# Kernel optimization log

Hardware: AMD Instinct MI355X
Metric: run time of the kernel (lower is better)

## Reference

```python
import jax, jax.numpy as jnp
import numpy as np

N_NODES = 100_000
N_EDGES = 1_600_000
N_FEAT = 64
HIDDEN = 64
BIOPRINT = 2048
N_GRAPHS = 1024


def setup_inputs() -> dict:
    key = jax.random.key(0)
    ks = jax.random.split(key, 12)
    x = jax.random.normal(ks[0], (N_NODES, N_FEAT), jnp.float32)
    edge_index = jax.random.randint(ks[1], (2, N_EDGES), 0, N_NODES, dtype=jnp.int64)
    batch = jnp.sort(jax.random.randint(ks[2], (N_NODES,), 0, N_GRAPHS, dtype=jnp.int64))
    def lin(k, fan_in, fan_out):
        s = 1.0 / np.sqrt(fan_in)
        return jax.random.uniform(k, (fan_in, fan_out), jnp.float32, -s, s)
    W1 = lin(ks[3], N_FEAT, HIDDEN)
    b1 = jnp.zeros((HIDDEN,), jnp.float32)
    W2 = lin(ks[4], HIDDEN, HIDDEN)
    b2 = jnp.zeros((HIDDEN,), jnp.float32)
    W3 = lin(ks[5], HIDDEN, HIDDEN)
    b3 = jnp.zeros((HIDDEN,), jnp.float32)
    Wd = lin(ks[6], HIDDEN, BIOPRINT)
    bd = jax.random.uniform(ks[7], (BIOPRINT,), jnp.float32, -1.0 / np.sqrt(HIDDEN), 1.0 / np.sqrt(HIDDEN))
    return {"x": x, "edge_index": edge_index, "batch": batch,
            "W1": W1, "b1": b1, "W2": W2, "b2": b2, "W3": W3, "b3": b3,
            "Wd": Wd, "bd": bd}


def reference(x, edge_index, batch, W1, b1, W2, b2, W3, b3, Wd, bd):
    n = x.shape[0]
    src, dst = edge_index[0], edge_index[1]
    # GCN symmetric normalization with self-loops: deg = in-degree + 1
    ones_e = jnp.ones(src.shape[0], x.dtype)
    deg = jax.ops.segment_sum(ones_e, dst, num_segments=n) + 1.0
    dinv = jax.lax.rsqrt(deg)  # deg >= 1 always
    self_norm = (dinv * dinv)[:, None]
    edge_norm = (dinv[src] * dinv[dst])[:, None]

    def gcn_conv(h, W, b):
        hw = h @ W  # [N, out]
        agg = jax.ops.segment_sum(hw[src] * edge_norm, dst, num_segments=n)
        return agg + hw * self_norm + b  # self-loop handled analytically

    h = jax.nn.relu(gcn_conv(x, W1, b1))
    h = jax.nn.relu(gcn_conv(h, W2, b2))
    h = gcn_conv(h, W3, b3)

    # global_mean_pool over graph ids
    cnt = jax.ops.segment_sum(jnp.ones(n, x.dtype), batch, num_segments=N_GRAPHS)
    pooled = jax.ops.segment_sum(h, batch, num_segments=N_GRAPHS) / jnp.maximum(cnt, 1.0)[:, None]

    # dropout(p=0.5) is identity in eval mode
    logits = pooled @ Wd + bd
    probs = jax.nn.softmax(logits, axis=-1)
    return (probs >= 0.5).astype(x.dtype)
```

## Files before the change

kernel.cpp:

```cpp
#include <hip/hip_runtime.h>
#include <hip/hip_fp16.h>
#include <math.h>

#define N_NODES   100000
#define N_EDGES   1600000
#define N_FEAT    64
#define HIDDEN    64
#define BIOPRINT  2048
#define N_GRAPHS  1024

#define SENTINEL  N_NODES
#define ELL_STRIDE 64

#define N_E4 (N_EDGES / 4)
#define FILL_BLOCKS ((N_E4 + 255) / 256)
#define MM1_BLOCKS (N_NODES / 32)
#define GS_BLOCKS  5

#define XCD_SLICE 12500
#define CHUNK_SHIFT 15
#define CH4 (1 << (CHUNK_SHIFT - 2))
#define NC 49
#define SLOT_P 56
#define CNT_BLOCKS (8 * SLOT_P)
#define PREP_BLOCKS ((N_NODES + 255) / 256)

typedef unsigned short u16;
typedef unsigned char  u8;

__device__ __forceinline__ __half2 shx_h2(__half2 v, int m) {
    int x = __shfl_xor(*(int*)&v, m);
    return *(__half2*)&x;
}

__device__ __forceinline__ void stage_w_perm(const float* __restrict__ W, float* sW, int t) {
    const float4* W4 = (const float4*)W;
    for (int i = t; i < 1024; i += 256) {
        float4 w = W4[i];
        int k = i >> 4;
        int c4 = (i & 15) * 4;
        int base = (k >> 2) * 256 + (k & 3);
        sW[base + (c4 + 0) * 4] = w.x;
        sW[base + (c4 + 1) * 4] = w.y;
        sW[base + (c4 + 2) * 4] = w.z;
        sW[base + (c4 + 3) * 4] = w.w;
    }
}

__global__ __launch_bounds__(256) void k_countmm(
        const int* __restrict__ dst, u16* __restrict__ counts, u8* __restrict__ rankl,
        const float* __restrict__ x, const float* __restrict__ W,
        __half* __restrict__ hw) {
    __shared__ int smem[XCD_SLICE];
    int bid = blockIdx.x, t = threadIdx.x;
    if (bid < CNT_BLOCKS) {
        int p = bid / SLOT_P;
        int c = bid % SLOT_P;
        if (c >= NC) return;
        int* hist = smem;
        for (int i = t; i < XCD_SLICE; i += 256) hist[i] = 0;
        __syncthreads();
        int lo = p * XCD_SLICE, hi = lo + XCD_SLICE;
        int base4 = c * CH4;
        int end4 = base4 + CH4; if (end4 > N_E4) end4 = N_E4;
        const int4* dst4 = (const int4*)dst;
        for (int i4 = base4 + t; i4 < end4; i4 += 256) {
            int4 d4 = dst4[i4];
            int e = i4 * 4;
            if (d4.x >= lo && d4.x < hi) rankl[e + 0] = (u8)atomicAdd(&hist[d4.x - lo], 1);
            if (d4.y >= lo && d4.y < hi) rankl[e + 1] = (u8)atomicAdd(&hist[d4.y - lo], 1);
            if (d4.z >= lo && d4.z < hi) rankl[e + 2] = (u8)atomicAdd(&hist[d4.z - lo], 1);
            if (d4.w >= lo && d4.w < hi) rankl[e + 3] = (u8)atomicAdd(&hist[d4.w - lo], 1);
        }
        __syncthreads();
        u16* crow = counts + (size_t)c * N_NODES + lo;
        for (int i = t; i < XCD_SLICE; i += 256) crow[i] = (u16)hist[i];
        return;
    }
    bid -= CNT_BLOCKS;
    float* sW = (float*)smem;
    float* sA = (float*)smem + 4096;
    stage_w_perm(W, sW, t);
    int row0 = bid * 32;
    ((float4*)sA)[t]       = ((const float4*)x)[row0 * 16 + t];
    ((float4*)sA)[t + 256] = ((const float4*)x)[row0 * 16 + t + 256];
    __syncthreads();
    int wave = t >> 6, lane = t & 63;
    const float4* sWp = (const float4*)sW;
    float sum[8] = {0.f, 0.f, 0.f, 0.f, 0.f, 0.f, 0.f, 0.f};
#pragma unroll
    for (int k4 = 0; k4 < 16; ++k4) {
        float4 w4 = sWp[k4 * 64 + lane];
#pragma unroll
        for (int hh = 0; hh < 8; ++hh) {
            float4 a4 = ((const float4*)&sA[(wave * 8 + hh) * 64])[k4];
            sum[hh] = fmaf(a4.x, w4.x, sum[hh]);
            sum[hh] = fmaf(a4.y, w4.y, sum[hh]);
            sum[hh] = fmaf(a4.z, w4.z, sum[hh]);
            sum[hh] = fmaf(a4.w, w4.w, sum[hh]);
        }
    }
#pragma unroll
    for (int hh = 0; hh < 8; ++hh) {
        int row = row0 + wave * 8 + hh;
        hw[(size_t)row * 64 + lane] = __float2half_rn(sum[hh]);
    }
}

__global__ __launch_bounds__(256) void k_prep(
        u16* __restrict__ counts, int* __restrict__ deg, float* __restrict__ dinv,
        const int* __restrict__ batch, int* __restrict__ gstart) {
    int bid = blockIdx.x, t = threadIdx.x;
    if (bid < PREP_BLOCKS) {
        int n = bid * 256 + t;
        if (n >= N_NODES) return;
        int s = 0;
#pragma unroll
        for (int c = 0; c < NC; ++c) {
            size_t idx = (size_t)c * N_NODES + n;
            int v = counts[idx];
            counts[idx] = (u16)s;
            s += v;
        }
        deg[n] = s;
        dinv[n] = rsqrtf((float)s + 1.0f);
        return;
    }
    int g = (bid - PREP_BLOCKS) * 256 + t;
    if (g > N_GRAPHS) return;
    if (g == N_GRAPHS) { gstart[g] = N_NODES; return; }
    int lo = 0, hi = N_NODES;
    while (lo < hi) { int mid = (lo + hi) >> 1; if (batch[mid] < g) lo = mid + 1; else hi = mid; }
    gstart[g] = lo;
}

__global__ __launch_bounds__(256) void k_fillscale(
        const int* __restrict__ src, const int* __restrict__ dst,
        const u8* __restrict__ rankl, const u16* __restrict__ counts,
        int* __restrict__ colELL,
        const int* __restrict__ deg, const float* __restrict__ dinv,
        __half* __restrict__ hw) {
    int bid = blockIdx.x, t = threadIdx.x;
    if (bid < FILL_BLOCKS) {
        int tid = bid * 256 + t;
        if (tid < N_E4) {
            int e = tid * 4;
            const u16* pref = counts + (size_t)(e >> CHUNK_SHIFT) * N_NODES;
            int4 d4 = ((const int4*)dst)[tid];
            uchar4 r4 = ((const uchar4*)rankl)[tid];
            int4 s4 = ((const int4*)src)[tid];
            int px = pref[d4.x] + r4.x; colELL[d4.x * ELL_STRIDE + (px & 63)] = s4.x;
            int py = pref[d4.y] + r4.y; colELL[d4.y * ELL_STRIDE + (py & 63)] = s4.y;
            int pz = pref[d4.z] + r4.z; colELL[d4.z * ELL_STRIDE + (pz & 63)] = s4.z;
            int pw = pref[d4.w] + r4.w; colELL[d4.w * ELL_STRIDE + (pw & 63)] = s4.w;
        }
        return;
    }
    bid -= FILL_BLOCKS;
    int row0 = bid * 32;
    int row = row0 + (t >> 3);
    float di = dinv[row];
    uint4* p = (uint4*)hw;
    uint4 v = p[(size_t)row * 8 + (t & 7)];
    __half2* h2 = (__half2*)&v;
#pragma unroll
    for (int c = 0; c < 4; ++c) {
        float2 f = __half22float2(h2[c]);
        h2[c] = __halves2half2(__float2half_rn(f.x * di), __float2half_rn(f.y * di));
    }
    p[(size_t)row * 8 + (t & 7)] = v;
    if (t < 32) {
        int r2 = row0 + t;
        int dv = deg[r2]; if (dv > 64) dv = 64;
        int vp = (dv + 15) & ~15;
        for (int j = dv; j < vp; ++j) colELL[r2 * ELL_STRIDE + j] = SENTINEL;
    }
}

__device__ __forceinline__ void gather2x8(
        const int* __restrict__ col, const uint4* __restrict__ hv,
        int rs, int re, int slot, int sub, float f[8]) {
    __half2 a0 = __float2half2_rn(0.f), a1 = a0, a2 = a0, a3 = a0;
    __half2 c0 = a0, c1 = a0, c2 = a0, c3 = a0;
    for (int e = rs; e < re; e += 16) {
        int s0 = __builtin_nontemporal_load(&col[e + slot]);
        int s1 = __builtin_nontemporal_load(&col[e + 2 + slot]);
        int s2 = __builtin_nontemporal_load(&col[e + 4 + slot]);
        int s3 = __builtin_nontemporal_load(&col[e + 6 + slot]);
        int s4 = __builtin_nontemporal_load(&col[e + 8 + slot]);
        int s5 = __builtin_nontemporal_load(&col[e + 10 + slot]);
        int s6 = __builtin_nontemporal_load(&col[e + 12 + slot]);
        int s7 = __builtin_nontemporal_load(&col[e + 14 + slot]);
        uint4 u0 = hv[(size_t)s0 * 8 + sub];
        uint4 u1 = hv[(size_t)s1 * 8 + sub];
        uint4 u2 = hv[(size_t)s2 * 8 + sub];
        uint4 u3 = hv[(size_t)s3 * 8 + sub];
        uint4 u4 = hv[(size_t)s4 * 8 + sub];
        uint4 u5 = hv[(size_t)s5 * 8 + sub];
        uint4 u6 = hv[(size_t)s6 * 8 + sub];
        uint4 u7 = hv[(size_t)s7 * 8 + sub];
        a0 = __hadd2(a0, *(__half2*)&u0.x); a1 = __hadd2(a1, *(__half2*)&u0.y);
        a2 = __hadd2(a2, *(__half2*)&u0.z); a3 = __hadd2(a3, *(__half2*)&u0.w);
        c0 = __hadd2(c0, *(__half2*)&u1.x); c1 = __hadd2(c1, *(__half2*)&u1.y);
        c2 = __hadd2(c2, *(__half2*)&u1.z); c3 = __hadd2(c3, *(__half2*)&u1.w);
        a0 = __hadd2(a0, *(__half2*)&u2.x); a1 = __hadd2(a1, *(__half2*)&u2.y);
        a2 = __hadd2(a2, *(__half2*)&u2.z); a3 = __hadd2(a3, *(__half2*)&u2.w);
        c0 = __hadd2(c0, *(__half2*)&u3.x); c1 = __hadd2(c1, *(__half2*)&u3.y);
        c2 = __hadd2(c2, *(__half2*)&u3.z); c3 = __hadd2(c3, *(__half2*)&u3.w);
        a0 = __hadd2(a0, *(__half2*)&u4.x); a1 = __hadd2(a1, *(__half2*)&u4.y);
        a2 = __hadd2(a2, *(__half2*)&u4.z); a3 = __hadd2(a3, *(__half2*)&u4.w);
        c0 = __hadd2(c0, *(__half2*)&u5.x); c1 = __hadd2(c1, *(__half2*)&u5.y);
        c2 = __hadd2(c2, *(__half2*)&u5.z); c3 = __hadd2(c3, *(__half2*)&u5.w);
        a0 = __hadd2(a0, *(__half2*)&u6.x); a1 = __hadd2(a1, *(__half2*)&u6.y);
        a2 = __hadd2(a2, *(__half2*)&u6.z); a3 = __hadd2(a3, *(__half2*)&u6.w);
        c0 = __hadd2(c0, *(__half2*)&u7.x); c1 = __hadd2(c1, *(__half2*)&u7.y);
        c2 = __hadd2(c2, *(__half2*)&u7.z); c3 = __hadd2(c3, *(__half2*)&u7.w);
    }
    a0 = __hadd2(a0, c0); a1 = __hadd2(a1, c1);
    a2 = __hadd2(a2, c2); a3 = __hadd2(a3, c3);
    a0 = __hadd2(a0, shx_h2(a0, 8));
    a1 = __hadd2(a1, shx_h2(a1, 8));
    a2 = __hadd2(a2, shx_h2(a2, 8));
    a3 = __hadd2(a3, shx_h2(a3, 8));
    float2 f0 = __half22float2(a0), f1 = __half22float2(a1);
    float2 f2 = __half22float2(a2), f3 = __half22float2(a3);
    f[0] = f0.x; f[1] = f0.y; f[2] = f1.x; f[3] = f1.y;
    f[4] = f2.x; f[5] = f2.y; f[6] = f3.x; f[7] = f3.y;
}

__global__ __launch_bounds__(256) void k_gmm(
        const int* __restrict__ deg, const int* __restrict__ col,
        const float* __restrict__ dinv, const float* __restrict__ b,
        const __half* __restrict__ hw_in, const float* __restrict__ W,
        __half* __restrict__ hw_out) {
    __shared__ float sW[64 * 64];
    __shared__ float sA[16 * 64];
    int t = threadIdx.x;
    stage_w_perm(W, sW, t);
    __syncthreads();

    int wave = t >> 6, lane = t & 63;
    int quarter = lane >> 4, slot = (lane >> 3) & 1, sub = lane & 7;
    int i0 = blockIdx.x * 16 + wave * 4;
    int i = i0 + quarter;
    float di = dinv[i];
    int dv = deg[i]; if (dv > 64) dv = 64;
    int rs = i * ELL_STRIDE;
    int re = rs + ((dv + 15) & ~15);
    const uint4* hv = (const uint4*)hw_in;

    float f[8];
    gather2x8(col, hv, rs, re, slot, sub, f);

    uint4 us = hv[(size_t)i * 8 + sub];
    float2 s0 = __half22float2(*(__half2*)&us.x);
    float2 s1 = __half22float2(*(__half2*)&us.y);
    float2 s2 = __half22float2(*(__half2*)&us.z);
    float2 s3 = __half22float2(*(__half2*)&us.w);
    float sf[8] = {s0.x, s0.y, s1.x, s1.y, s2.x, s2.y, s3.x, s3.y};
    float4 ba = ((const float4*)b)[sub * 2];
    float4 bb = ((const float4*)b)[sub * 2 + 1];
    float bf[8] = {ba.x, ba.y, ba.z, ba.w, bb.x, bb.y, bb.z, bb.w};
    if (slot == 0) {
        float r[8];
#pragma unroll
        for (int k = 0; k < 8; ++k) r[k] = fmaxf(fmaf(di, f[k] + sf[k], bf[k]), 0.f);
        *(float4*)&sA[(wave * 4 + quarter) * 64 + sub * 8]     = make_float4(r[0], r[1], r[2], r[3]);
        *(float4*)&sA[(wave * 4 + quarter) * 64 + sub * 8 + 4] = make_float4(r[4], r[5], r[6], r[7]);
    }

    const float4* sWp = (const float4*)sW;
    float sum[4] = {0.f, 0.f, 0.f, 0.f};
#pragma unroll
    for (int k4 = 0; k4 < 16; ++k4) {
        float4 w4 = sWp[k4 * 64 + lane];
#pragma unroll
        for (int hh = 0; hh < 4; ++hh) {
            float4 a4 = ((const float4*)&sA[(wave * 4 + hh) * 64])[k4];
            sum[hh] = fmaf(a4.x, w4.x, sum[hh]);
            sum[hh] = fmaf(a4.y, w4.y, sum[hh]);
            sum[hh] = fmaf(a4.z, w4.z, sum[hh]);
            sum[hh] = fmaf(a4.w, w4.w, sum[hh]);
        }
    }
#pragma unroll
    for (int hh = 0; hh < 4; ++hh)
        hw_out[(size_t)(i0 + hh) * 64 + lane] = __float2half_rn(sum[hh] * dinv[i0 + hh]);
}

__global__ __launch_bounds__(256) void k_gather3(
        const int* __restrict__ deg, const int* __restrict__ col,
        const float* __restrict__ dinv, const float* __restrict__ b,
        const __half* __restrict__ hw_in, __half* __restrict__ conv) {
    int t = threadIdx.x;
    int wave = t >> 6, lane = t & 63;
    int quarter = lane >> 4, slot = (lane >> 3) & 1, sub = lane & 7;
    int i = blockIdx.x * 16 + wave * 4 + quarter;
    float di = dinv[i];
    int dv = deg[i]; if (dv > 64) dv = 64;
    int rs = i * ELL_STRIDE;
    int re = rs + ((dv + 15) & ~15);
    const uint4* hv = (const uint4*)hw_in;

    float f[8];
    gather2x8(col, hv, rs, re, slot, sub, f);

    if (slot == 0) {
        uint4 us = hv[(size_t)i * 8 + sub];
        float2 s0 = __half22float2(*(__half2*)&us.x);
        float2 s1 = __half22float2(*(__half2*)&us.y);
        float2 s2 = __half22float2(*(__half2*)&us.z);
        float2 s3 = __half22float2(*(__half2*)&us.w);
        float sf[8] = {s0.x, s0.y, s1.x, s1.y, s2.x, s2.y, s3.x, s3.y};
        float4 ba = ((const float4*)b)[sub * 2];
        float4 bb = ((const float4*)b)[sub * 2 + 1];
        float bf[8] = {ba.x, ba.y, ba.z, ba.w, bb.x, bb.y, bb.z, bb.w};
        uint4 o;
        __half2* oh = (__half2*)&o;
#pragma unroll
        for (int c = 0; c < 4; ++c) {
            float r0 = fmaf(di, f[2 * c] + sf[2 * c], bf[2 * c]);
            float r1 = fmaf(di, f[2 * c + 1] + sf[2 * c + 1], bf[2 * c + 1]);
            oh[c] = __halves2half2(__float2half_rn(r0), __float2half_rn(r1));
        }
        ((uint4*)conv)[(size_t)i * 8 + sub] = o;
    }
}

__global__ __launch_bounds__(256) void k_dense(
        const __half* __restrict__ conv, const int* __restrict__ gstart,
        const float* __restrict__ Wd, const float* __restrict__ bd,
        float* __restrict__ out) {
    __shared__ float sred[4][64];
    __shared__ float sp[64];
    __shared__ float rmax[4];
    __shared__ float rsum[4];
    int t = threadIdx.x;
    int wave = t >> 6, lane = t & 63;
    int g = blockIdx.x;
    int n0 = gstart[g], n1 = gstart[g + 1];

    int fp = lane & 31;
    int par = lane >> 5;
    const __half2* conv2 = (const __half2*)conv;
    float2 acc2 = make_float2(0.f, 0.f);
    for (int i = n0 + wave * 2 + par; i < n1; i += 8) {
        float2 f = __half22float2(conv2[(size_t)i * 32 + fp]);
        acc2.x += f.x; acc2.y += f.y;
    }
    acc2.x += __shfl_xor(acc2.x, 32);
    acc2.y += __shfl_xor(acc2.y, 32);
    if (lane < 32) { sred[wave][2 * fp] = acc2.x; sred[wave][2 * fp + 1] = acc2.y; }
    __syncthreads();
    if (t < 64) {
        int n = n1 - n0;
        float s = sred[0][t] + sred[1][t] + sred[2][t] + sred[3][t];
        sp[t] = (n > 0) ? s / (float)n : 0.f;
    }
    __syncthreads();

    float acc[8];
#pragma unroll
    for (int r = 0; r < 8; ++r) acc[r] = bd[r * 256 + t];
    for (int k = 0; k < 64; ++k) {
        float h = sp[k];
#pragma unroll
        for (int r = 0; r < 8; ++r)
            acc[r] = fmaf(h, Wd[k * BIOPRINT + r * 256 + t], acc[r]);
    }

    float m = acc[0];
#pragma unroll
    for (int r = 1; r < 8; ++r) m = fmaxf(m, acc[r]);
#pragma unroll
    for (int off = 32; off > 0; off >>= 1) m = fmaxf(m, __shfl_xor(m, off));
    if (lane == 0) rmax[wave] = m;
    __syncthreads();
    m = fmaxf(fmaxf(rmax[0], rmax[1]), fmaxf(rmax[2], rmax[3]));

    float s = 0.f;
#pragma unroll
    for (int r = 0; r < 8; ++r) { acc[r] = expf(acc[r] - m); s += acc[r]; }
#pragma unroll
    for (int off = 32; off > 0; off >>= 1) s += __shfl_xor(s, off);
    if (lane == 0) rsum[wave] = s;
    __syncthreads();
    s = rsum[0] + rsum[1] + rsum[2] + rsum[3];

#pragma unroll
    for (int r = 0; r < 8; ++r) {
        float p = acc[r] / s;
        out[(size_t)g * BIOPRINT + r * 256 + t] = (p >= 0.5f) ? 1.0f : 0.0f;
    }
}


extern "C" void kernel_launch(void* const* d_in, const int* in_sizes, int n_in,
                              void* d_out, int out_size, void* d_ws, size_t ws_size,
                              hipStream_t stream) {
    const float* x     = (const float*)d_in[0];
    const int*   ei    = (const int*)d_in[1];
    const int*   batch = (const int*)d_in[2];
    const float* W1 = (const float*)d_in[3];
    const float* b1 = (const float*)d_in[4];
    const float* W2 = (const float*)d_in[5];
    const float* b2 = (const float*)d_in[6];
    const float* W3 = (const float*)d_in[7];
    const float* b3 = (const float*)d_in[8];
    const float* Wd = (const float*)d_in[9];
    const float* bd = (const float*)d_in[10];
    float* out = (float*)d_out;

    const int* src = ei;
    const int* dst = ei + N_EDGES;

    char* ws = (char*)d_ws;
    size_t off = 0;
    auto alloc = [&](size_t bytes) {
        void* p = ws + off;
        off += (bytes + 255) & ~(size_t)255;
        return p;
    };
    int*    deg    = (int*)alloc(N_NODES * sizeof(int));
    float*  dinv   = (float*)alloc(N_NODES * sizeof(float));
    u8*     rankl  = (u8*)alloc((size_t)N_EDGES * sizeof(u8));
    int*    gstart = (int*)alloc((N_GRAPHS + 1) * sizeof(int));
    u16*    counts = (u16*)alloc((size_t)NC * N_NODES * sizeof(u16));
    int*    colELL = (int*)alloc((size_t)N_NODES * ELL_STRIDE * sizeof(int));
    __half* bufA   = (__half*)alloc((size_t)(N_NODES + 1) * HIDDEN * sizeof(__half));
    __half* bufB   = (__half*)alloc((size_t)(N_NODES + 1) * HIDDEN * sizeof(__half));
    __half* conv   = (__half*)alloc((size_t)N_NODES * HIDDEN * sizeof(__half));

    hipMemsetAsync(bufA + (size_t)N_NODES * HIDDEN, 0, HIDDEN * sizeof(__half), stream);
    hipMemsetAsync(bufB + (size_t)N_NODES * HIDDEN, 0, HIDDEN * sizeof(__half), stream);

    k_countmm<<<CNT_BLOCKS + MM1_BLOCKS, 256, 0, stream>>>(dst, counts, rankl, x, W1, bufA);
    k_prep<<<PREP_BLOCKS + GS_BLOCKS, 256, 0, stream>>>(counts, deg, dinv, batch, gstart);
    k_fillscale<<<FILL_BLOCKS + MM1_BLOCKS, 256, 0, stream>>>(
        src, dst, rankl, counts, colELL, deg, dinv, bufA);

    const int g16_grid = N_NODES / 16;
    k_gmm<<<g16_grid, 256, 0, stream>>>(deg, colELL, dinv, b1, bufA, W2, bufB);
    k_gmm<<<g16_grid, 256, 0, stream>>>(deg, colELL, dinv, b2, bufB, W3, bufA);
    k_gather3<<<g16_grid, 256, 0, stream>>>(deg, colELL, dinv, b3, bufA, conv);
    k_dense<<<N_GRAPHS, 256, 0, stream>>>(conv, gstart, Wd, bd, out);
}
```

Before: 309.2 us.

## Partition ELL fill by XCD node slice with prefix offsets staged in LDS

```diff
diff --git a/kernel.cpp b/kernel.cpp
--- a/kernel.cpp
+++ b/kernel.cpp
@@ -13,7 +13,6 @@
 #define ELL_STRIDE 64
 
 #define N_E4 (N_EDGES / 4)
-#define FILL_BLOCKS ((N_E4 + 255) / 256)
 #define MM1_BLOCKS (N_NODES / 32)
 #define GS_BLOCKS  5
 
@@ -23,6 +22,7 @@
 #define NC 49
 #define SLOT_P 56
 #define CNT_BLOCKS (8 * SLOT_P)
+#define FILL_BLOCKS (8 * SLOT_P)
 #define PREP_BLOCKS ((N_NODES + 255) / 256)
 
 typedef unsigned short u16;
@@ -108,7 +108,8 @@
 }
 
 __global__ __launch_bounds__(256) void k_prep(
-        u16* __restrict__ counts, int* __restrict__ deg, float* __restrict__ dinv,
+        const u16* __restrict__ counts, u8* __restrict__ pref8,
+        int* __restrict__ deg, float* __restrict__ dinv,
         const int* __restrict__ batch, int* __restrict__ gstart) {
     int bid = blockIdx.x, t = threadIdx.x;
     if (bid < PREP_BLOCKS) {
@@ -119,7 +120,7 @@
         for (int c = 0; c < NC; ++c) {
             size_t idx = (size_t)c * N_NODES + n;
             int v = counts[idx];
-            counts[idx] = (u16)s;
+            pref8[idx] = (u8)s;
             s += v;
         }
         deg[n] = s;
@@ -136,23 +137,46 @@
 
 __global__ __launch_bounds__(256) void k_fillscale(
         const int* __restrict__ src, const int* __restrict__ dst,
-        const u8* __restrict__ rankl, const u16* __restrict__ counts,
+        const u8* __restrict__ rankl, const u8* __restrict__ pref8,
         int* __restrict__ colELL,
         const int* __restrict__ deg, const float* __restrict__ dinv,
         __half* __restrict__ hw) {
+    __shared__ u8 spref[XCD_SLICE];
     int bid = blockIdx.x, t = threadIdx.x;
     if (bid < FILL_BLOCKS) {
-        int tid = bid * 256 + t;
-        if (tid < N_E4) {
-            int e = tid * 4;
-            const u16* pref = counts + (size_t)(e >> CHUNK_SHIFT) * N_NODES;
-            int4 d4 = ((const int4*)dst)[tid];
-            uchar4 r4 = ((const uchar4*)rankl)[tid];
-            int4 s4 = ((const int4*)src)[tid];
-            int px = pref[d4.x] + r4.x; colELL[d4.x * ELL_STRIDE + (px & 63)] = s4.x;
-            int py = pref[d4.y] + r4.y; colELL[d4.y * ELL_STRIDE + (py & 63)] = s4.y;
-            int pz = pref[d4.z] + r4.z; colELL[d4.z * ELL_STRIDE + (pz & 63)] = s4.z;
-            int pw = pref[d4.w] + r4.w; colELL[d4.w * ELL_STRIDE + (pw & 63)] = s4.w;
+        int p = bid / SLOT_P;
+        int c = bid % SLOT_P;
+        if (c >= NC) return;
+        const u8* prow = pref8 + (size_t)c * N_NODES + p * XCD_SLICE;
+        for (int i = t; i < XCD_SLICE / 4; i += 256)
+            ((uchar4*)spref)[i] = ((const uchar4*)prow)[i];
+        __syncthreads();
+        int lo = p * XCD_SLICE, hi = lo + XCD_SLICE;
+        int base4 = c * CH4;
+        int end4 = base4 + CH4; if (end4 > N_E4) end4 = N_E4;
+        const int4* dst4 = (const int4*)dst;
+        const int4* src4 = (const int4*)src;
+        const uchar4* rank4 = (const uchar4*)rankl;
+        for (int i4 = base4 + t; i4 < end4; i4 += 256) {
+            int4 d4 = dst4[i4];
+            int4 s4 = src4[i4];
+            uchar4 r4 = rank4[i4];
+            if (d4.x >= lo && d4.x < hi) {
+                int sl = spref[d4.x - lo] + r4.x;
+                colELL[d4.x * ELL_STRIDE + (sl & 63)] = s4.x;
+            }
+            if (d4.y >= lo && d4.y < hi) {
+                int sl = spref[d4.y - lo] + r4.y;
+                colELL[d4.y * ELL_STRIDE + (sl & 63)] = s4.y;
+            }
+            if (d4.z >= lo && d4.z < hi) {
+                int sl = spref[d4.z - lo] + r4.z;
+                colELL[d4.z * ELL_STRIDE + (sl & 63)] = s4.z;
+            }
+            if (d4.w >= lo && d4.w < hi) {
+                int sl = spref[d4.w - lo] + r4.w;
+                colELL[d4.w * ELL_STRIDE + (sl & 63)] = s4.w;
+            }
         }
         return;
     }
@@ -426,6 +450,7 @@
     u8*     rankl  = (u8*)alloc((size_t)N_EDGES * sizeof(u8));
     int*    gstart = (int*)alloc((N_GRAPHS + 1) * sizeof(int));
     u16*    counts = (u16*)alloc((size_t)NC * N_NODES * sizeof(u16));
+    u8*     pref8  = (u8*)alloc((size_t)NC * N_NODES * sizeof(u8));
     int*    colELL = (int*)alloc((size_t)N_NODES * ELL_STRIDE * sizeof(int));
     __half* bufA   = (__half*)alloc((size_t)(N_NODES + 1) * HIDDEN * sizeof(__half));
     __half* bufB   = (__half*)alloc((size_t)(N_NODES + 1) * HIDDEN * sizeof(__half));
@@ -435,9 +460,9 @@
     hipMemsetAsync(bufB + (size_t)N_NODES * HIDDEN, 0, HIDDEN * sizeof(__half), stream);
 
     k_countmm<<<CNT_BLOCKS + MM1_BLOCKS, 256, 0, stream>>>(dst, counts, rankl, x, W1, bufA);
-    k_prep<<<PREP_BLOCKS + GS_BLOCKS, 256, 0, stream>>>(counts, deg, dinv, batch, gstart);
+    k_prep<<<PREP_BLOCKS + GS_BLOCKS, 256, 0, stream>>>(counts, pref8, deg, dinv, batch, gstart);
     k_fillscale<<<FILL_BLOCKS + MM1_BLOCKS, 256, 0, stream>>>(
-        src, dst, rankl, counts, colELL, deg, dinv, bufA);
+        src, dst, rankl, pref8, colELL, deg, dinv, bufA);
 
     const int g16_grid = N_NODES / 16;
     k_gmm<<<g16_grid, 256, 0, stream>>>(deg, colELL, dinv, b1, bufA, W2, bufB);
```

Result: slower. 327.5 us (+5.9%).
